# Kernel tuning notes

Measured on AMD Instinct MI355X. Metric: run time of the kernel, lower is better.

The kernel has to match this reference:

```python
import jax, jax.numpy as jnp
import numpy as np

N_HOPS = 3
N_USERS = 50000
N_ITEMS = 50000
N = N_USERS + N_ITEMS
NNZ = 3200000
D = 64
EDGE_DROP = 0.5   # note: torch floor(rate+rand) trick KEEPS edges with prob = rate
MESS_DROP = 0.1


def setup_inputs() -> dict:
    key = jax.random.key(0)
    k1, k2, k3, k4, k5 = jax.random.split(key, 5)
    user_embed = jax.random.normal(k1, (N_USERS, D), dtype=jnp.float32)
    item_embed = jax.random.normal(k2, (N_ITEMS, D), dtype=jnp.float32)
    edge_rows = jax.random.randint(k3, (NNZ,), 0, N, dtype=jnp.int32)
    edge_cols = jax.random.randint(k4, (NNZ,), 0, N, dtype=jnp.int32)
    edge_vals = jax.random.uniform(k5, (NNZ,), dtype=jnp.float32)
    return {"user_embed": user_embed, "item_embed": item_embed,
            "edge_vals": edge_vals, "edge_rows": edge_rows, "edge_cols": edge_cols}


def reference(user_embed, item_embed, edge_vals, edge_rows, edge_cols):
    # forward path: mess_dropout=True, edge_dropout=True, perturbed=False
    all_embed = jnp.concatenate([user_embed, item_embed], axis=0)  # [N, D]
    agg = all_embed
    embs = [all_embed]
    base_key = jax.random.key(42)
    for hop in range(N_HOPS):
        ke, km = jax.random.split(jax.random.fold_in(base_key, hop))
        # sparse edge dropout: torch floor(rate + U[0,1)) == 1 <=> U >= 1-rate
        keep = jax.random.uniform(ke, (NNZ,)) >= (1.0 - EDGE_DROP)
        v = jnp.where(keep, edge_vals, 0.0) * (1.0 / (1.0 - EDGE_DROP))  # [NNZ]
        # SpMM via gather + segment_sum (zeroed values == dropped edges)
        msgs = v[:, None] * agg[edge_cols]                                # [NNZ, D]
        agg = jax.ops.segment_sum(msgs, edge_rows, num_segments=N)       # [N, D]
        # message (dense) dropout, inverted scaling like nn.Dropout
        mmask = jax.random.bernoulli(km, 1.0 - MESS_DROP, agg.shape)
        agg = agg * mmask.astype(agg.dtype) * (1.0 / (1.0 - MESS_DROP))
        embs.append(agg)
    embs = jnp.stack(embs, axis=1)  # [N, N_HOPS+1, D]
    return embs[:N_USERS], embs[N_USERS:]
```

## Files before the change

### kernel.cpp

```cpp
#include <hip/hip_runtime.h>
#include <cstdint>

namespace {
constexpr int kNUsers = 50000;
constexpr int kNTotal = 100000;
constexpr int kD = 64;
constexpr int kHops = 3;
constexpr int kNnz = 3200000;
constexpr int kRowStride = (kHops + 1) * kD;
constexpr uint32_t kColMask = (1u << 17) - 1u;
constexpr int kSBShift = 7;
constexpr int kSBRows = 1 << kSBShift;
constexpr int kNSB = (kNTotal + kSBRows - 1) / kSBRows;
constexpr int kSBCap = 5120;
constexpr int kP1Batch = 16384;
constexpr int kP1Blocks = (kNnz + kP1Batch - 1) / kP1Batch;
constexpr int kP1Threads = 1024;
constexpr int kEPT = kP1Batch / kP1Threads;
}

#define ROTL32(v, r) (((v) << (r)) | ((v) >> (32 - (r))))

__host__ __device__ inline void tf2x32(uint32_t k0, uint32_t k1,
                                       uint32_t &x0, uint32_t &x1) {
  const uint32_t k2 = k0 ^ k1 ^ 0x1BD11BDAu;
  x0 += k0; x1 += k1;
#define TFR(r) { x0 += x1; x1 = ROTL32(x1, r); x1 ^= x0; }
  TFR(13) TFR(15) TFR(26) TFR(6)
  x0 += k1; x1 += k2 + 1u;
  TFR(17) TFR(29) TFR(16) TFR(24)
  x0 += k2; x1 += k0 + 2u;
  TFR(13) TFR(15) TFR(26) TFR(6)
  x0 += k0; x1 += k1 + 3u;
  TFR(17) TFR(29) TFR(16) TFR(24)
  x0 += k1; x1 += k2 + 4u;
  TFR(13) TFR(15) TFR(26) TFR(6)
  x0 += k2; x1 += k0 + 5u;
#undef TFR
}

__device__ __forceinline__ uint32_t pbits(uint32_t k0, uint32_t k1, uint32_t i) {
  uint32_t x0 = 0u, x1 = i;
  tf2x32(k0, k1, x0, x1);
  return x0 ^ x1;
}

__device__ __forceinline__ float u01(uint32_t b) {
  return __uint_as_float((b >> 9) | 0x3f800000u) - 1.0f;
}

__global__ void k_init(const float* __restrict__ ue, const float* __restrict__ ie,
                       float* __restrict__ out, int* __restrict__ tail) {
  int t = blockIdx.x * blockDim.x + threadIdx.x;
  if (t < kNSB) tail[t] = 0;
  if (t >= kNTotal * 16) return;
  int n = t >> 4, c = t & 15;
  float4 v = (n < kNUsers) ? reinterpret_cast<const float4*>(ue)[n * 16 + c]
                           : reinterpret_cast<const float4*>(ie)[(n - kNUsers) * 16 + c];
  reinterpret_cast<float4*>(out)[(size_t)n * (kRowStride / 4) + c] = v;
}

__global__ __launch_bounds__(1024) void k_split1(
    const int* __restrict__ er, const int* __restrict__ ec,
    const float* __restrict__ ev, int* __restrict__ tail,
    int2* __restrict__ stage,
    uint32_t ke0_0, uint32_t ke1_0, uint32_t ke0_1, uint32_t ke1_1,
    uint32_t ke0_2, uint32_t ke1_2) {
  __shared__ int hist[kNSB];
  __shared__ int base[kNSB];
  const int t = threadIdx.x;
  const int e0 = blockIdx.x * kP1Batch;
  const int n = min(kP1Batch, kNnz - e0);
  for (int i = t; i < kNSB; i += kP1Threads) hist[i] = 0;
  __syncthreads();
  int rr[kEPT];
#pragma unroll
  for (int j = 0; j < kEPT; ++j) {
    const int i = j * kP1Threads + t;
    rr[j] = (i < n) ? __builtin_nontemporal_load(er + e0 + i) : -1;
    if (rr[j] >= 0) atomicAdd(&hist[(uint32_t)rr[j] >> kSBShift], 1);
  }
  __syncthreads();
  for (int i = t; i < kNSB; i += kP1Threads) {
    const int c = hist[i];
    base[i] = (c > 0) ? atomicAdd(&tail[i], c) : 0;
    hist[i] = 0;
  }
  __syncthreads();
#pragma unroll
  for (int j = 0; j < kEPT; ++j) {
    if (rr[j] < 0) continue;
    const int e = e0 + j * kP1Threads + t;
    const int b = (uint32_t)rr[j] >> kSBShift;
    const int pos = base[b] + atomicAdd(&hist[b], 1);
    if (pos < kSBCap) {
      uint32_t x = (uint32_t)__builtin_nontemporal_load(ec + e);
      const float v = __builtin_nontemporal_load(ev + e);
      if (u01(pbits(ke0_0, ke1_0, (uint32_t)e)) >= 0.5f) x |= 1u << 17;
      if (u01(pbits(ke0_1, ke1_1, (uint32_t)e)) >= 0.5f) x |= 1u << 18;
      if (u01(pbits(ke0_2, ke1_2, (uint32_t)e)) >= 0.5f) x |= 1u << 19;
      x |= (uint32_t)(rr[j] & (kSBRows - 1)) << 20;
      stage[(size_t)b * kSBCap + pos] = make_int2((int)x, __float_as_int(v * 2.0f));
    }
  }
}

__global__ __launch_bounds__(256) void k_split2(
    const int* __restrict__ tail, int2* __restrict__ stage,
    int* __restrict__ row_start, int* __restrict__ row_len) {
  __shared__ int2 st[kSBCap];
  __shared__ int lcnt[kSBRows], lsc[kSBRows], lcur[kSBRows];
  const int b = blockIdx.x;
  const int t = threadIdx.x;
  const int row0 = b << kSBShift;
  const int nrows = min(kSBRows, kNTotal - row0);
  const int n = min(tail[b], kSBCap);
  int2* reg = stage + (size_t)b * kSBCap;
  if (t < kSBRows) { lcnt[t] = 0; lcur[t] = 0; }
  for (int i = t; i < n; i += 256) st[i] = reg[i];
  __syncthreads();
  for (int i = t; i < n; i += 256)
    atomicAdd(&lcnt[((uint32_t)st[i].x >> 20) & (kSBRows - 1u)], 1);
  __syncthreads();
  if (t < kSBRows) lsc[t] = lcnt[t];
  __syncthreads();
  for (int off = 1; off < kSBRows; off <<= 1) {
    int add = (t >= off && t < kSBRows) ? lsc[t - off] : 0;
    __syncthreads();
    if (t < kSBRows) lsc[t] += add;
    __syncthreads();
  }
  if (t < nrows) {
    const int excl = lsc[t] - lcnt[t];
    row_start[row0 + t] = b * kSBCap + excl;
    row_len[row0 + t] = lcnt[t];
  }
  __syncthreads();
  for (int i = t; i < n; i += 256) {
    const int2 v = st[i];
    const int r = (int)(((uint32_t)v.x >> 20) & (kSBRows - 1u));
    const int pos = (lsc[r] - lcnt[r]) + atomicAdd(&lcur[r], 1);
    reg[pos] = v;
  }
}

__device__ __forceinline__ float4 fma4(float4 a, float s, float4 g) {
  a.x += s * g.x; a.y += s * g.y; a.z += s * g.z; a.w += s * g.w;
  return a;
}

__global__ __launch_bounds__(256) void k_spmm_csr(
    const int* __restrict__ row_start, const int* __restrict__ row_len,
    const int2* __restrict__ csr,
    const float* __restrict__ src, float* __restrict__ dst,
    uint32_t hopbit, uint32_t km0, uint32_t km1) {
  __shared__ int2 stage[4][80];
  const int wave = threadIdx.x >> 6;
  const int lane = threadIdx.x & 63;
  const int grp  = lane >> 4;
  const int sub  = lane & 15;
  const int r = __builtin_amdgcn_readfirstlane(blockIdx.x * 4 + wave);
  if (r >= kNTotal) return;
  const int start = row_start[r];
  const int end = start + row_len[r];
  float4 ac0 = make_float4(0.f, 0.f, 0.f, 0.f);
  float4 ac1 = make_float4(0.f, 0.f, 0.f, 0.f);
  float4 ac2 = make_float4(0.f, 0.f, 0.f, 0.f);
  float4 ac3 = make_float4(0.f, 0.f, 0.f, 0.f);
  for (int base = start; base < end; base += 64) {
    const int n = min(64, end - base);
    bool keep = false;
    int2 cv = make_int2(0, 0);
    if (lane < n) {
      cv = csr[base + lane];
      keep = ((uint32_t)cv.x & hopbit) != 0u;
    }
    const uint64_t m = __ballot(keep);
    const int k = __popcll(m);
    if (keep) {
      const int slot = __popcll(m & ((1ull << lane) - 1ull));
      stage[wave][slot] = make_int2((int)((uint32_t)cv.x & kColMask), cv.y);
    }
    if (lane < 15) stage[wave][k + lane] = make_int2(0, 0);
    for (int j = 0; j < k; j += 16) {
      const int2 e0 = stage[wave][j + grp];
      const int2 e1 = stage[wave][j + 4 + grp];
      const int2 e2 = stage[wave][j + 8 + grp];
      const int2 e3 = stage[wave][j + 12 + grp];
      const float4 g0 = *reinterpret_cast<const float4*>(
          src + (size_t)e0.x * kRowStride + (sub << 2));
      const float4 g1 = *reinterpret_cast<const float4*>(
          src + (size_t)e1.x * kRowStride + (sub << 2));
      const float4 g2 = *reinterpret_cast<const float4*>(
          src + (size_t)e2.x * kRowStride + (sub << 2));
      const float4 g3 = *reinterpret_cast<const float4*>(
          src + (size_t)e3.x * kRowStride + (sub << 2));
      ac0 = fma4(ac0, __int_as_float(e0.y), g0);
      ac1 = fma4(ac1, __int_as_float(e1.y), g1);
      ac2 = fma4(ac2, __int_as_float(e2.y), g2);
      ac3 = fma4(ac3, __int_as_float(e3.y), g3);
    }
  }
  float4 a;
  a.x = (ac0.x + ac1.x) + (ac2.x + ac3.x);
  a.y = (ac0.y + ac1.y) + (ac2.y + ac3.y);
  a.z = (ac0.z + ac1.z) + (ac2.z + ac3.z);
  a.w = (ac0.w + ac1.w) + (ac2.w + ac3.w);
  a.x += __shfl_xor(a.x, 16); a.y += __shfl_xor(a.y, 16);
  a.z += __shfl_xor(a.z, 16); a.w += __shfl_xor(a.w, 16);
  a.x += __shfl_xor(a.x, 32); a.y += __shfl_xor(a.y, 32);
  a.z += __shfl_xor(a.z, 32); a.w += __shfl_xor(a.w, 32);
  const int srcl = lane >> 2;
  const float c0 = __shfl(a.x, srcl);
  const float c1 = __shfl(a.y, srcl);
  const float c2 = __shfl(a.z, srcl);
  const float c3 = __shfl(a.w, srcl);
  const float acc = (lane & 2) ? ((lane & 1) ? c3 : c2)
                               : ((lane & 1) ? c1 : c0);
  const float u = u01(pbits(km0, km1, (uint32_t)(r * 64 + lane)));
  dst[(size_t)r * kRowStride + lane] = (u < 0.9f) ? acc * (float)(1.0 / 0.9) : 0.0f;
}

extern "C" void kernel_launch(void* const* d_in, const int* in_sizes, int n_in,
                              void* d_out, int out_size, void* d_ws, size_t ws_size,
                              hipStream_t stream) {
  const float* ue = (const float*)d_in[0];
  const float* ie = (const float*)d_in[1];
  const float* ev = (const float*)d_in[2];
  const int*   er = (const int*)d_in[3];
  const int*   ec = (const int*)d_in[4];
  float* out = (float*)d_out;

  uint32_t ke0[kHops], ke1[kHops], km0[kHops], km1[kHops];
  for (int hop = 0; hop < kHops; ++hop) {
    uint32_t f0 = 0u, f1 = (uint32_t)hop;
    tf2x32(0u, 42u, f0, f1);
    uint32_t e0 = 0u, e1 = 0u;
    tf2x32(f0, f1, e0, e1);
    uint32_t m0 = 0u, m1 = 1u;
    tf2x32(f0, f1, m0, m1);
    ke0[hop] = e0; ke1[hop] = e1;
    km0[hop] = m0; km1[hop] = m1;
  }

  const int BS = 256;

  const size_t off_rowstart = 0;
  const size_t off_rowlen   = 100000;
  const size_t off_tail     = 200000;
  const size_t off_stage    = 200784;
  int*  row_start = (int*)d_ws + off_rowstart;
  int*  row_len   = (int*)d_ws + off_rowlen;
  int*  tail      = (int*)d_ws + off_tail;
  int2* stage     = (int2*)((int*)d_ws + off_stage);

  k_init<<<(kNTotal * 16 + BS - 1) / BS, BS, 0, stream>>>(ue, ie, out, tail);
  k_split1<<<kP1Blocks, kP1Threads, 0, stream>>>(
      er, ec, ev, tail, stage,
      ke0[0], ke1[0], ke0[1], ke1[1], ke0[2], ke1[2]);
  k_split2<<<kNSB, 256, 0, stream>>>(tail, stage, row_start, row_len);

  for (int hop = 0; hop < kHops; ++hop) {
    const float* src = out + (size_t)hop * kD;
    float*       dst = out + (size_t)(hop + 1) * kD;
    k_spmm_csr<<<(kNTotal + 3) / 4, 256, 0, stream>>>(
        row_start, row_len, stage, src, dst, 1u << (17 + hop), km0[hop], km1[hop]);
  }
}
```

Measured before the change: 282.0 us.

## Stage bucketed edges in LDS before coalesced writes in split pass

```diff
diff --git a/kernel.cpp b/kernel.cpp
--- a/kernel.cpp
+++ b/kernel.cpp
@@ -13,7 +13,7 @@
 constexpr int kSBRows = 1 << kSBShift;
 constexpr int kNSB = (kNTotal + kSBRows - 1) / kSBRows;
 constexpr int kSBCap = 5120;
-constexpr int kP1Batch = 16384;
+constexpr int kP1Batch = 6144;
 constexpr int kP1Blocks = (kNnz + kP1Batch - 1) / kP1Batch;
 constexpr int kP1Threads = 1024;
 constexpr int kEPT = kP1Batch / kP1Threads;
@@ -66,8 +66,10 @@
     int2* __restrict__ stage,
     uint32_t ke0_0, uint32_t ke1_0, uint32_t ke0_1, uint32_t ke1_1,
     uint32_t ke0_2, uint32_t ke1_2) {
+  __shared__ int2 ent[kP1Batch];
   __shared__ int hist[kNSB];
-  __shared__ int base[kNSB];
+  __shared__ int lbase[kNSB];
+  __shared__ int gbase[kNSB];
   const int t = threadIdx.x;
   const int e0 = blockIdx.x * kP1Batch;
   const int n = min(kP1Batch, kNnz - e0);
@@ -81,10 +83,19 @@
     if (rr[j] >= 0) atomicAdd(&hist[(uint32_t)rr[j] >> kSBShift], 1);
   }
   __syncthreads();
-  for (int i = t; i < kNSB; i += kP1Threads) {
-    const int c = hist[i];
-    base[i] = (c > 0) ? atomicAdd(&tail[i], c) : 0;
-    hist[i] = 0;
+  if (t < kNSB) lbase[t] = hist[t];
+  __syncthreads();
+  for (int off = 1; off < kNSB; off <<= 1) {
+    int add = (t >= off && t < kNSB) ? lbase[t - off] : 0;
+    __syncthreads();
+    if (t < kNSB) lbase[t] += add;
+    __syncthreads();
+  }
+  if (t < kNSB) {
+    const int c = hist[t];
+    lbase[t] -= c;
+    gbase[t] = (c > 0) ? atomicAdd(&tail[t], c) : 0;
+    hist[t] = 0;
   }
   __syncthreads();
 #pragma unroll
@@ -92,20 +103,29 @@
     if (rr[j] < 0) continue;
     const int e = e0 + j * kP1Threads + t;
     const int b = (uint32_t)rr[j] >> kSBShift;
-    const int pos = base[b] + atomicAdd(&hist[b], 1);
-    if (pos < kSBCap) {
-      uint32_t x = (uint32_t)__builtin_nontemporal_load(ec + e);
-      const float v = __builtin_nontemporal_load(ev + e);
-      if (u01(pbits(ke0_0, ke1_0, (uint32_t)e)) >= 0.5f) x |= 1u << 17;
-      if (u01(pbits(ke0_1, ke1_1, (uint32_t)e)) >= 0.5f) x |= 1u << 18;
-      if (u01(pbits(ke0_2, ke1_2, (uint32_t)e)) >= 0.5f) x |= 1u << 19;
-      x |= (uint32_t)(rr[j] & (kSBRows - 1)) << 20;
-      stage[(size_t)b * kSBCap + pos] = make_int2((int)x, __float_as_int(v * 2.0f));
-    }
-  }
-}
-
-__global__ __launch_bounds__(256) void k_split2(
+    uint32_t x = (uint32_t)__builtin_nontemporal_load(ec + e);
+    const float v = __builtin_nontemporal_load(ev + e);
+    if (u01(pbits(ke0_0, ke1_0, (uint32_t)e)) >= 0.5f) x |= 1u << 17;
+    if (u01(pbits(ke0_1, ke1_1, (uint32_t)e)) >= 0.5f) x |= 1u << 18;
+    if (u01(pbits(ke0_2, ke1_2, (uint32_t)e)) >= 0.5f) x |= 1u << 19;
+    x |= (uint32_t)(rr[j] & (kSBRows - 1)) << 20;
+    const int pos = lbase[b] + atomicAdd(&hist[b], 1);
+    ent[pos] = make_int2((int)x, __float_as_int(v * 2.0f));
+  }
+  __syncthreads();
+  for (int i = t; i < n; i += kP1Threads) {
+    int lo = 0, hi = kNSB - 1;
+    while (lo < hi) {
+      const int mid = (lo + hi + 1) >> 1;
+      if (lbase[mid] <= i) lo = mid; else hi = mid - 1;
+    }
+    const int idx = gbase[lo] + (i - lbase[lo]);
+    if (idx < kSBCap)
+      stage[(size_t)lo * kSBCap + idx] = ent[i];
+  }
+}
+
+__global__ __launch_bounds__(512) void k_split2(
     const int* __restrict__ tail, int2* __restrict__ stage,
     int* __restrict__ row_start, int* __restrict__ row_len) {
   __shared__ int2 st[kSBCap];
@@ -117,9 +137,9 @@
   const int n = min(tail[b], kSBCap);
   int2* reg = stage + (size_t)b * kSBCap;
   if (t < kSBRows) { lcnt[t] = 0; lcur[t] = 0; }
-  for (int i = t; i < n; i += 256) st[i] = reg[i];
-  __syncthreads();
-  for (int i = t; i < n; i += 256)
+  for (int i = t; i < n; i += 512) st[i] = reg[i];
+  __syncthreads();
+  for (int i = t; i < n; i += 512)
     atomicAdd(&lcnt[((uint32_t)st[i].x >> 20) & (kSBRows - 1u)], 1);
   __syncthreads();
   if (t < kSBRows) lsc[t] = lcnt[t];
@@ -136,7 +156,7 @@
     row_len[row0 + t] = lcnt[t];
   }
   __syncthreads();
-  for (int i = t; i < n; i += 256) {
+  for (int i = t; i < n; i += 512) {
     const int2 v = st[i];
     const int r = (int)(((uint32_t)v.x >> 20) & (kSBRows - 1u));
     const int pos = (lsc[r] - lcnt[r]) + atomicAdd(&lcur[r], 1);
@@ -258,7 +278,7 @@
   k_split1<<<kP1Blocks, kP1Threads, 0, stream>>>(
       er, ec, ev, tail, stage,
       ke0[0], ke1[0], ke0[1], ke1[1], ke0[2], ke1[2]);
-  k_split2<<<kNSB, 256, 0, stream>>>(tail, stage, row_start, row_len);
+  k_split2<<<kNSB, 512, 0, stream>>>(tail, stage, row_start, row_len);
 
   for (int hop = 0; hop < kHops; ++hop) {
     const float* src = out + (size_t)hop * kD;
```

New measurement: 268.8 us. -4.7%, faster.
